# Kernel tuning notes

Measured on AMD Instinct MI355X. Metric: run time of the kernel, lower is better.

## Reference

```python
import jax, jax.numpy as jnp
import numpy as np

B = 65536      # batch size
H = 256        # hidden_size (args['hid_dim'])
MID = 300      # hard-coded encoder bottleneck in CommonFeatureExtractor
THR = 0.6      # similarity_threshold


def _lin(k, fin, fout):
    return jax.random.normal(k, (fin, fout), jnp.float32) / np.sqrt(fin)


def setup_inputs() -> dict:
    key = jax.random.key(0)
    ks = jax.random.split(key, 24)
    inp = {
        'brics': jax.random.normal(ks[0], (B, H), jnp.float32),
        'function_group': jax.random.normal(ks[1], (B, H), jnp.float32),
        'pharmacophore': jax.random.normal(ks[2], (B, H), jnp.float32),
    }
    # three fp encoders: Linear(H,300) -> ReLU -> (Dropout eval) -> Linear(300,H)
    for n, (k1, k2) in zip(['b', 'f', 'p'], [(ks[3], ks[4]), (ks[5], ks[6]), (ks[7], ks[8])]):
        inp['W1_' + n] = _lin(k1, H, MID)
        inp['b1_' + n] = jnp.zeros((MID,), jnp.float32)
        inp['W2_' + n] = _lin(k2, MID, H)
        inp['b2_' + n] = jnp.zeros((H,), jnp.float32)
    inp['Wg'] = _lin(ks[9], 3 * H, 3)        # weight_generator
    inp['bg_v'] = jnp.zeros((3,), jnp.float32)
    inp['We'] = _lin(ks[10], H, H)           # enhancement_layer
    inp['be_v'] = jnp.zeros((H,), jnp.float32)
    inp['Wf'] = _lin(ks[11], 2 * H, H)       # fusion_layer
    inp['bf_v'] = jnp.zeros((H,), jnp.float32)
    return inp


def _fwd(brics, function_group, pharmacophore,
         W1_b, b1_b, W2_b, b2_b, W1_f, b1_f, W2_f, b2_f, W1_p, b1_p, W2_p, b2_p,
         Wg, bg_v, We, be_v, Wf, bf_v):
    def enc(x, W1, b1, W2, b2):
        return jax.nn.relu(x @ W1 + b1) @ W2 + b2  # dropout in eval mode = identity

    eb = enc(brics, W1_b, b1_b, W2_b, b2_b)
    ef = enc(function_group, W1_f, b1_f, W2_f, b2_f)
    ep = enc(pharmacophore, W1_p, b1_p, W2_p, b2_p)

    fps = jnp.stack([eb, ef, ep], axis=1)                              # [B,3,H]
    fpn = fps / jnp.maximum(jnp.linalg.norm(fps, axis=-1, keepdims=True), 1e-12)

    # the 3 unordered pairs (0,1),(0,2),(1,2); the torch sort is irrelevant
    # because the selected pairs are combined by a permutation-invariant
    # softmax-weighted sum.
    ii = jnp.array([0, 0, 1])
    jj = jnp.array([1, 2, 2])
    elem = fpn[:, ii] * fpn[:, jj]                                     # [B,3,H]
    sims = elem.sum(-1)                                                # [B,3] cosine sims
    pmask = sims > THR
    common = 0.5 * (fps[:, ii] + fps[:, jj]) * (elem > THR)            # [B,3,H]

    has = pmask.any(-1)                                                # [B]
    m = jnp.max(jnp.where(pmask, sims, -jnp.inf), axis=-1, keepdims=True)
    m = jnp.where(jnp.isfinite(m), m, 0.0)
    e = jnp.where(pmask, jnp.exp(sims - m), 0.0)                       # masked softmax
    w = e / jnp.maximum(e.sum(-1, keepdims=True), 1e-12)
    sample_common = (common * w[..., None]).sum(1)                     # [B,H]
    common_features = jnp.where(has[:, None], sample_common, fps.mean(1))

    allc = jnp.concatenate([eb, ef, ep], axis=1)                       # [B,3H]
    fw = jax.nn.softmax(allc @ Wg + bg_v, axis=1)                      # [B,3]
    weighted = eb * fw[:, 0:1] + ef * fw[:, 1:2] + ep * fw[:, 2:3]

    enh = jax.nn.sigmoid(common_features @ We + be_v)
    fused = jnp.concatenate([weighted, common_features * enh], axis=1) @ Wf + bf_v
    return fused


def reference(brics, function_group, pharmacophore,
              W1_b, b1_b, W2_b, b2_b, W1_f, b1_f, W2_f, b2_f, W1_p, b1_p, W2_p, b2_p,
              Wg, bg_v, We, be_v, Wf, bf_v):
    return _fwd(brics, function_group, pharmacophore,
                W1_b, b1_b, W2_b, b2_b, W1_f, b1_f, W2_f, b2_f, W1_p, b1_p, W2_p, b2_p,
                Wg, bg_v, We, be_v, Wf, bf_v)
```

## Files before the change

kernel.cpp:

```cpp
#include <hip/hip_runtime.h>

typedef unsigned short u16;
typedef __bf16 bf16x8 __attribute__((ext_vector_type(8)));
typedef float f32x4 __attribute__((ext_vector_type(4)));
typedef unsigned short u16x8 __attribute__((ext_vector_type(8)));

__device__ __forceinline__ float b2f(u16 b){ union{unsigned u; float f;} v; v.u=((unsigned)b)<<16; return v.f; }
__device__ __forceinline__ u16 f2b(float f){ unsigned u=__builtin_bit_cast(unsigned,f); return (u16)((u+0x7fffu+((u>>16)&1u))>>16); }
__device__ __forceinline__ float wred32(float v){
  #pragma unroll
  for(int off=16; off>0; off>>=1) v += __shfl_xor(v, off, 64);
  return v;
}
__device__ __forceinline__ void stOut(u16* p, float v){ *p = f2b(v); }
__device__ __forceinline__ void stOut(float* p, float v){ *p = v; }

__device__ __forceinline__ void gload_lds16(const void* g, void* l){
  __builtin_amdgcn_global_load_lds(
      (const __attribute__((address_space(1))) void*)g,
      (__attribute__((address_space(3))) void*)l, 16, 0, 0);
}

template<int PER>
__device__ __forceinline__ void stage_tile_b16(const u16* __restrict__ base, int rstride,
                                               int kcol, u16* lds, int w, int lane){
  #pragma unroll
  for(int it=0; it<PER; ++it){
    int cbase = it*512 + w*64;
    int ch = cbase + lane;
    int r = ch >> 3;
    int ce = ((ch & 7) * 8) ^ ((r & 7) << 3);
    gload_lds16(base + (size_t)r*rstride + kcol + ce, lds + cbase*8);
  }
}

struct Af32Regs { float4 a0, b0, a1, b1; };
__device__ __forceinline__ void loadA_f32(Af32Regs& rg, const float* __restrict__ Ap,
                                          int lda, int kcol, int tid){
  {
    int ch = tid;       int r = ch>>3, s = (ch&7)*8;
    const float* src = Ap + (size_t)r*lda + kcol + s;
    rg.a0 = *(const float4*)src; rg.b0 = *(const float4*)(src+4);
  }
  {
    int ch = tid + 512; int r = ch>>3, s = (ch&7)*8;
    const float* src = Ap + (size_t)r*lda + kcol + s;
    rg.a1 = *(const float4*)src; rg.b1 = *(const float4*)(src+4);
  }
}
__device__ __forceinline__ void writeA_f32(const Af32Regs& rg, u16* As, int tid){
  {
    int ch = tid;       int r = ch>>3, s = (ch&7)*8;
    u16* dst = &As[r*64 + (s ^ ((r&7)<<3))];
    ushort4 o0{f2b(rg.a0.x),f2b(rg.a0.y),f2b(rg.a0.z),f2b(rg.a0.w)};
    ushort4 o1{f2b(rg.b0.x),f2b(rg.b0.y),f2b(rg.b0.z),f2b(rg.b0.w)};
    *(ushort4*)dst = o0; *(ushort4*)(dst+4) = o1;
  }
  {
    int ch = tid + 512; int r = ch>>3, s = (ch&7)*8;
    u16* dst = &As[r*64 + (s ^ ((r&7)<<3))];
    ushort4 o0{f2b(rg.a1.x),f2b(rg.a1.y),f2b(rg.a1.z),f2b(rg.a1.w)};
    ushort4 o1{f2b(rg.b1.x),f2b(rg.b1.y),f2b(rg.b1.z),f2b(rg.b1.w)};
    *(ushort4*)dst = o0; *(ushort4*)(dst+4) = o1;
  }
}

struct GP {
  const void* A[3];
  const void* A2;
  const u16*  Wt[3];
  const float* bias[3];
  void* C[3];
  const u16* mult;
  int lda, K, Nreal, ldc, ldm;
};

template<int MODE, typename OT, typename AT, bool DUAL, int NWT>
__global__ __launch_bounds__(512, 2) void gemm_w(GP p)
{
  const int z = blockIdx.z;
  const AT* __restrict__ A  = (const AT*)p.A[z];
  const AT* __restrict__ A2 = (const AT*)p.A2;
  const u16* __restrict__ Wt = p.Wt[z];
  const float* __restrict__ bias = p.bias[z];
  OT* __restrict__ C = (OT*)p.C[z];
  const int lda = p.lda, K = p.K, ldc = p.ldc;

  __shared__ __align__(16) u16 As[2][128*64];
  __shared__ __align__(16) u16 Bs[2][NWT*64*64];

  const int tid = threadIdx.x;
  const size_t m0 = (size_t)blockIdx.x * 128;
  const int lane = tid & 63, w = tid >> 6;
  const int lr = lane & 15, quad = lane >> 4;
  const int wr = (w >> 2) * 64, wc = (w & 3) * (NWT*16);
  const int swz = (lr & 7) << 3;
  const int KH = K >> 1, NT = K >> 6;

  f32x4 acc[4][NWT];
  #pragma unroll
  for(int i=0;i<4;++i)
    #pragma unroll
    for(int j=0;j<NWT;++j) acc[i][j] = (f32x4){0.f,0.f,0.f,0.f};

  const AT* Ab1 = A + m0*(size_t)lda;
  const AT* Ab2 = DUAL ? (A2 + m0*(size_t)lda) : nullptr;

  {
    if constexpr (__is_same(AT, u16)) {
      stage_tile_b16<2>((const u16*)Ab1, lda, 0, As[0], w, lane);
    } else {
      Af32Regs rg; loadA_f32(rg, (const float*)Ab1, lda, 0, tid);
      writeA_f32(rg, As[0], tid);
    }
    stage_tile_b16<NWT>(Wt, K, 0, Bs[0], w, lane);
  }
  __syncthreads();

  int cur = 0;
  for(int t=0; t<NT; ++t){
    const int knext = (t+1) << 6;
    const bool pf = (t+1) < NT;
    Af32Regs rg;
    if (pf){
      const AT* Ap = Ab1; int kc = knext;
      if (DUAL && knext >= KH) { Ap = Ab2; kc = knext - KH; }
      if constexpr (__is_same(AT, u16))
        stage_tile_b16<2>((const u16*)Ap, lda, kc, As[cur^1], w, lane);
      else
        loadA_f32(rg, (const float*)Ap, lda, kc, tid);
      stage_tile_b16<NWT>(Wt, K, knext, Bs[cur^1], w, lane);
    }
    #pragma unroll
    for(int kk=0; kk<64; kk+=32){
      bf16x8 af[4], bq[NWT];
      #pragma unroll
      for(int i=0;i<4;++i)
        af[i] = *(const bf16x8*)&As[cur][(wr + i*16 + lr)*64 + ((kk + quad*8) ^ swz)];
      #pragma unroll
      for(int j=0;j<NWT;++j)
        bq[j] = *(const bf16x8*)&Bs[cur][(wc + j*16 + lr)*64 + ((kk + quad*8) ^ swz)];
      #pragma unroll
      for(int i=0;i<4;++i)
        #pragma unroll
        for(int j=0;j<NWT;++j)
          acc[i][j] = __builtin_amdgcn_mfma_f32_16x16x32_bf16(af[i], bq[j], acc[i][j], 0, 0, 0);
    }
    if constexpr (!__is_same(AT, u16)) { if (pf) writeA_f32(rg, As[cur^1], tid); }
    __syncthreads();
    cur ^= 1;
  }

  #pragma unroll
  for(int j=0;j<NWT;++j){
    int col = wc + j*16 + lr;
    float bv = (col < p.Nreal) ? bias[col] : 0.f;
    #pragma unroll
    for(int i=0;i<4;++i){
      #pragma unroll
      for(int r=0;r<4;++r){
        size_t row = m0 + wr + i*16 + quad*4 + r;
        size_t ci = row*(size_t)ldc + col;
        float v = acc[i][j][r] + bv;
        if(MODE==1) v = fmaxf(v, 0.f);
        if(MODE==2){
          float mv = b2f(p.mult[row*(size_t)p.ldm + col]);
          v = mv * __builtin_amdgcn_rcpf(1.f + __expf(-v));
        }
        stOut(&C[ci], v);
      }
    }
  }
}

struct TPar { const float* src; u16* dst; int K, N, Kp, Np; };
struct TArgs { TPar p[8]; };
__global__ __launch_bounds__(256) void transpose_all(TArgs args){
  TPar p = args.p[blockIdx.y];
  int n = blockIdx.x;
  if (n >= p.Np) return;
  for (int k = threadIdx.x; k < p.Kp; k += 256){
    u16 v = 0;
    if (n < p.N && k < p.K) v = f2b(p.src[(size_t)k*p.N + n]);
    p.dst[(size_t)n*p.Kp + k] = v;
  }
}

__global__ __launch_bounds__(256) void mid_k(
    const u16* eb, const u16* ef, const u16* ep,
    const float* __restrict__ Wg, const float* __restrict__ bg,
    u16* common, u16* weighted)
{
  const int wid = threadIdx.x >> 6, lane = threadIdx.x & 63;
  const int half = lane >> 5, l5 = lane & 31;
  const size_t row = (size_t)blockIdx.x * 8 + wid*2 + half;
  const size_t base = row*256 + l5*8;

  u16x8 vb = *(const u16x8*)(eb + base);
  u16x8 vf = *(const u16x8*)(ef + base);
  u16x8 vp = *(const u16x8*)(ep + base);
  float fb[8], ff[8], fp[8];
  #pragma unroll
  for(int j=0;j<8;++j){ fb[j]=b2f(vb[j]); ff[j]=b2f(vf[j]); fp[j]=b2f(vp[j]); }

  float sb=0, sf=0, sp=0, d01=0, d02=0, d12=0, g0=0, g1=0, g2=0;
  #pragma unroll
  for(int j=0;j<8;++j){
    sb += fb[j]*fb[j]; sf += ff[j]*ff[j]; sp += fp[j]*fp[j];
    d01 += fb[j]*ff[j]; d02 += fb[j]*fp[j]; d12 += ff[j]*fp[j];
  }
  #pragma unroll
  for(int seg=0; seg<3; ++seg){
    const float* x = (seg==0) ? fb : (seg==1) ? ff : fp;
    const float* wg = Wg + ((size_t)seg*256 + l5*8)*3;
    float wv[24];
    #pragma unroll
    for(int q=0;q<6;++q){
      float4 t = *(const float4*)(wg + q*4);
      wv[q*4+0]=t.x; wv[q*4+1]=t.y; wv[q*4+2]=t.z; wv[q*4+3]=t.w;
    }
    #pragma unroll
    for(int j=0;j<8;++j){
      g0 += x[j]*wv[j*3+0];
      g1 += x[j]*wv[j*3+1];
      g2 += x[j]*wv[j*3+2];
    }
  }
  sb=wred32(sb); sf=wred32(sf); sp=wred32(sp);
  d01=wred32(d01); d02=wred32(d02); d12=wred32(d12);
  g0=wred32(g0); g1=wred32(g1); g2=wred32(g2);

  float inb  = __builtin_amdgcn_rsqf(fmaxf(sb, 1e-24f));
  float invf = __builtin_amdgcn_rsqf(fmaxf(sf, 1e-24f));
  float inp  = __builtin_amdgcn_rsqf(fmaxf(sp, 1e-24f));
  float s01 = d01*inb*invf, s02 = d02*inb*inp, s12 = d12*invf*inp;

  g0 += bg[0]; g1 += bg[1]; g2 += bg[2];
  float gm = fmaxf(g0, fmaxf(g1, g2));
  float e0 = __expf(g0-gm), e1 = __expf(g1-gm), e2 = __expf(g2-gm);
  float res = __builtin_amdgcn_rcpf(e0+e1+e2);
  float fw0 = e0*res, fw1 = e1*res, fw2 = e2*res;

  bool p0 = s01 > 0.6f, p1 = s02 > 0.6f, p2 = s12 > 0.6f;
  bool has = p0 || p1 || p2;
  float mm = -__builtin_inff();
  if(p0) mm = fmaxf(mm, s01);
  if(p1) mm = fmaxf(mm, s02);
  if(p2) mm = fmaxf(mm, s12);
  if(!has) mm = 0.f;
  float q0 = p0 ? __expf(s01-mm) : 0.f;
  float q1 = p1 ? __expf(s02-mm) : 0.f;
  float q2 = p2 ? __expf(s12-mm) : 0.f;
  float rqs = __builtin_amdgcn_rcpf(fmaxf(q0+q1+q2, 1e-12f));
  float w0 = q0*rqs, w1 = q1*rqs, w2 = q2*rqs;

  u16x8 oc, ow;
  #pragma unroll
  for(int j=0;j<8;++j){
    float a = fb[j], b = ff[j], c = fp[j];
    float na = a*inb, nbv = b*invf, nc = c*inp;
    float c0 = (na*nbv > 0.6f) ? 0.5f*(a+b) : 0.f;
    float c1 = (na*nc  > 0.6f) ? 0.5f*(a+c) : 0.f;
    float c2 = (nbv*nc > 0.6f) ? 0.5f*(b+c) : 0.f;
    float sc = c0*w0 + c1*w1 + c2*w2;
    float cf = has ? sc : (a+b+c)*(1.f/3.f);
    float wv = a*fw0 + b*fw1 + c*fw2;
    oc[j] = f2b(cf); ow[j] = f2b(wv);
  }
  *(u16x8*)(common + base) = oc;
  *(u16x8*)(weighted + base) = ow;
}

extern "C" void kernel_launch(void* const* d_in, const int* in_sizes, int n_in,
                              void* d_out, int out_size, void* d_ws, size_t ws_size,
                              hipStream_t stream) {
  const float* brics = (const float*)d_in[0];
  const float* fg    = (const float*)d_in[1];
  const float* ph    = (const float*)d_in[2];
  const float* W1[3] = {(const float*)d_in[3], (const float*)d_in[7], (const float*)d_in[11]};
  const float* b1[3] = {(const float*)d_in[4], (const float*)d_in[8], (const float*)d_in[12]};
  const float* W2[3] = {(const float*)d_in[5], (const float*)d_in[9], (const float*)d_in[13]};
  const float* b2[3] = {(const float*)d_in[6], (const float*)d_in[10], (const float*)d_in[14]};
  const float* Wg = (const float*)d_in[15];
  const float* bg = (const float*)d_in[16];
  const float* We = (const float*)d_in[17];
  const float* be = (const float*)d_in[18];
  const float* Wf = (const float*)d_in[19];
  const float* bf = (const float*)d_in[20];
  float* out = (float*)d_out;

  const int M = in_sizes[0] / 256;

  char* wsp = (char*)d_ws;
  size_t off = 0;
  auto carve = [&](size_t elems)->u16* {
    u16* p = (u16*)(wsp + off);
    off += ((elems*sizeof(u16)) + 255) & ~(size_t)255;
    return p;
  };
  u16* xb0 = carve((size_t)M*256);
  u16* xb1 = carve((size_t)M*256);
  u16* xb2 = carve((size_t)M*256);
  u16* Wt1[3], *Wt2[3];
  for(int i=0;i<3;++i) Wt1[i] = carve(320*256);
  for(int i=0;i<3;++i) Wt2[i] = carve(256*320);
  u16* WtE = carve(256*256);
  u16* WtF = carve(256*512);

  size_t hb = (((size_t)M*320*sizeof(u16)) + 255) & ~(size_t)255;
  bool batched = (off + 3*hb) <= ws_size;
  u16* hh[3];
  hh[0] = (u16*)(wsp + off);
  hh[1] = batched ? (u16*)(wsp + off + hb)   : hh[0];
  hh[2] = batched ? (u16*)(wsp + off + 2*hb) : hh[0];
  (void)n_in; (void)out_size;

  TArgs ta;
  for(int i=0;i<3;++i){
    ta.p[i]   = {W1[i], Wt1[i], 256, 300, 256, 320};
    ta.p[3+i] = {W2[i], Wt2[i], 300, 256, 320, 256};
  }
  ta.p[6] = {We, WtE, 256, 256, 256, 256};
  ta.p[7] = {Wf, WtF, 512, 256, 512, 256};
  transpose_all<<<dim3(512, 8), 256, 0, stream>>>(ta);

  const float* xin[3] = {brics, fg, ph};
  u16* encp[3] = {xb0, xb1, xb2};
  if (batched) {
    GP g1{};
    for(int i=0;i<3;++i){ g1.A[i]=xin[i]; g1.Wt[i]=Wt1[i]; g1.bias[i]=b1[i]; g1.C[i]=hh[i]; }
    g1.lda=256; g1.K=256; g1.Nreal=300; g1.ldc=320;
    gemm_w<1,u16,float,false,5><<<dim3(M/128, 1, 3), 512, 0, stream>>>(g1);
    GP g2{};
    for(int i=0;i<3;++i){ g2.A[i]=hh[i]; g2.Wt[i]=Wt2[i]; g2.bias[i]=b2[i]; g2.C[i]=encp[i]; }
    g2.lda=320; g2.K=320; g2.Nreal=256; g2.ldc=256;
    gemm_w<0,u16,u16,false,4><<<dim3(M/128, 1, 3), 512, 0, stream>>>(g2);
  } else {
    for(int i=0;i<3;++i){
      GP g1{}; g1.A[0]=xin[i]; g1.Wt[0]=Wt1[i]; g1.bias[0]=b1[i]; g1.C[0]=hh[0];
      g1.lda=256; g1.K=256; g1.Nreal=300; g1.ldc=320;
      gemm_w<1,u16,float,false,5><<<dim3(M/128, 1, 1), 512, 0, stream>>>(g1);
      GP g2{}; g2.A[0]=hh[0]; g2.Wt[0]=Wt2[i]; g2.bias[0]=b2[i]; g2.C[0]=encp[i];
      g2.lda=320; g2.K=320; g2.Nreal=256; g2.ldc=256;
      gemm_w<0,u16,u16,false,4><<<dim3(M/128, 1, 1), 512, 0, stream>>>(g2);
    }
  }

  mid_k<<<M/8, 256, 0, stream>>>(xb0, xb1, xb2, Wg, bg, xb2, xb0);

  {
    GP gg{}; gg.A[0]=xb2; gg.Wt[0]=WtE; gg.bias[0]=be; gg.C[0]=xb1;
    gg.mult=xb2; gg.lda=256; gg.K=256; gg.Nreal=256; gg.ldc=256; gg.ldm=256;
    gemm_w<2,u16,u16,false,4><<<dim3(M/128, 1, 1), 512, 0, stream>>>(gg);
  }

  {
    GP gf{}; gf.A[0]=xb0; gf.A2=xb1; gf.Wt[0]=WtF; gf.bias[0]=bf; gf.C[0]=out;
    gf.lda=256; gf.K=512; gf.Nreal=256; gf.ldc=256;
    gemm_w<0,float,u16,true,4><<<dim3(M/128, 1, 1), 512, 0, stream>>>(gf);
  }
}
```

Measured before the change: 497.5 us.

## Fuse similarity/mix, enhancement GEMM and fusion GEMM into one kernel

```diff
diff --git a/kernel.cpp b/kernel.cpp
--- a/kernel.cpp
+++ b/kernel.cpp
@@ -12,8 +12,6 @@
   for(int off=16; off>0; off>>=1) v += __shfl_xor(v, off, 64);
   return v;
 }
-__device__ __forceinline__ void stOut(u16* p, float v){ *p = f2b(v); }
-__device__ __forceinline__ void stOut(float* p, float v){ *p = v; }
 
 __device__ __forceinline__ void gload_lds16(const void* g, void* l){
   __builtin_amdgcn_global_load_lds(
@@ -67,27 +65,26 @@
 
 struct GP {
   const void* A[3];
-  const void* A2;
   const u16*  Wt[3];
   const float* bias[3];
   void* C[3];
-  const u16* mult;
-  int lda, K, Nreal, ldc, ldm;
+  int lda, K, Nreal, ldc;
 };
 
-template<int MODE, typename OT, typename AT, bool DUAL, int NWT>
+template<int MODE, typename AT, int NWT>
 __global__ __launch_bounds__(512, 2) void gemm_w(GP p)
 {
+  constexpr int BN = NWT*64;
+  constexpr int AHALF = 128*64;
+  constexpr int BHALF = BN*64;
+  __shared__ __align__(16) u16 smem[2*AHALF + 2*BHALF];
+
   const int z = blockIdx.z;
   const AT* __restrict__ A  = (const AT*)p.A[z];
-  const AT* __restrict__ A2 = (const AT*)p.A2;
   const u16* __restrict__ Wt = p.Wt[z];
   const float* __restrict__ bias = p.bias[z];
-  OT* __restrict__ C = (OT*)p.C[z];
+  u16* __restrict__ C = (u16*)p.C[z];
   const int lda = p.lda, K = p.K, ldc = p.ldc;
-
-  __shared__ __align__(16) u16 As[2][128*64];
-  __shared__ __align__(16) u16 Bs[2][NWT*64*64];
 
   const int tid = threadIdx.x;
   const size_t m0 = (size_t)blockIdx.x * 128;
@@ -95,7 +92,7 @@
   const int lr = lane & 15, quad = lane >> 4;
   const int wr = (w >> 2) * 64, wc = (w & 3) * (NWT*16);
   const int swz = (lr & 7) << 3;
-  const int KH = K >> 1, NT = K >> 6;
+  const int NT = K >> 6;
 
   f32x4 acc[4][NWT];
   #pragma unroll
@@ -103,18 +100,15 @@
     #pragma unroll
     for(int j=0;j<NWT;++j) acc[i][j] = (f32x4){0.f,0.f,0.f,0.f};
 
-  const AT* Ab1 = A + m0*(size_t)lda;
-  const AT* Ab2 = DUAL ? (A2 + m0*(size_t)lda) : nullptr;
-
-  {
-    if constexpr (__is_same(AT, u16)) {
-      stage_tile_b16<2>((const u16*)Ab1, lda, 0, As[0], w, lane);
-    } else {
-      Af32Regs rg; loadA_f32(rg, (const float*)Ab1, lda, 0, tid);
-      writeA_f32(rg, As[0], tid);
-    }
-    stage_tile_b16<NWT>(Wt, K, 0, Bs[0], w, lane);
-  }
+  const AT* Ab = A + m0*(size_t)lda;
+
+  if constexpr (__is_same(AT, u16)) {
+    stage_tile_b16<2>((const u16*)Ab, lda, 0, smem, w, lane);
+  } else {
+    Af32Regs rg; loadA_f32(rg, (const float*)Ab, lda, 0, tid);
+    writeA_f32(rg, smem, tid);
+  }
+  stage_tile_b16<NWT>(Wt, K, 0, smem + 2*AHALF, w, lane);
   __syncthreads();
 
   int cur = 0;
@@ -123,34 +117,37 @@
     const bool pf = (t+1) < NT;
     Af32Regs rg;
     if (pf){
-      const AT* Ap = Ab1; int kc = knext;
-      if (DUAL && knext >= KH) { Ap = Ab2; kc = knext - KH; }
       if constexpr (__is_same(AT, u16))
-        stage_tile_b16<2>((const u16*)Ap, lda, kc, As[cur^1], w, lane);
+        stage_tile_b16<2>((const u16*)Ab, lda, knext, smem + (cur^1)*AHALF, w, lane);
       else
-        loadA_f32(rg, (const float*)Ap, lda, kc, tid);
-      stage_tile_b16<NWT>(Wt, K, knext, Bs[cur^1], w, lane);
-    }
+        loadA_f32(rg, (const float*)Ab, lda, knext, tid);
+      stage_tile_b16<NWT>(Wt, K, knext, smem + 2*AHALF + (cur^1)*BHALF, w, lane);
+    }
+    const u16* Asc = smem + cur*AHALF;
+    const u16* Bsc = smem + 2*AHALF + cur*BHALF;
     #pragma unroll
     for(int kk=0; kk<64; kk+=32){
       bf16x8 af[4], bq[NWT];
       #pragma unroll
       for(int i=0;i<4;++i)
-        af[i] = *(const bf16x8*)&As[cur][(wr + i*16 + lr)*64 + ((kk + quad*8) ^ swz)];
+        af[i] = *(const bf16x8*)&Asc[(wr + i*16 + lr)*64 + ((kk + quad*8) ^ swz)];
       #pragma unroll
       for(int j=0;j<NWT;++j)
-        bq[j] = *(const bf16x8*)&Bs[cur][(wc + j*16 + lr)*64 + ((kk + quad*8) ^ swz)];
+        bq[j] = *(const bf16x8*)&Bsc[(wc + j*16 + lr)*64 + ((kk + quad*8) ^ swz)];
       #pragma unroll
       for(int i=0;i<4;++i)
         #pragma unroll
         for(int j=0;j<NWT;++j)
           acc[i][j] = __builtin_amdgcn_mfma_f32_16x16x32_bf16(af[i], bq[j], acc[i][j], 0, 0, 0);
     }
-    if constexpr (!__is_same(AT, u16)) { if (pf) writeA_f32(rg, As[cur^1], tid); }
+    if constexpr (!__is_same(AT, u16)) { if (pf) writeA_f32(rg, smem + (cur^1)*AHALF, tid); }
     __syncthreads();
     cur ^= 1;
   }
 
+  constexpr int BNP = BN + 8;
+  static_assert(128*BNP <= 2*AHALF + 2*BHALF, "Ct fits in smem");
+  u16* Ct = smem;
   #pragma unroll
   for(int j=0;j<NWT;++j){
     int col = wc + j*16 + lr;
@@ -159,17 +156,19 @@
     for(int i=0;i<4;++i){
       #pragma unroll
       for(int r=0;r<4;++r){
-        size_t row = m0 + wr + i*16 + quad*4 + r;
-        size_t ci = row*(size_t)ldc + col;
         float v = acc[i][j][r] + bv;
         if(MODE==1) v = fmaxf(v, 0.f);
-        if(MODE==2){
-          float mv = b2f(p.mult[row*(size_t)p.ldm + col]);
-          v = mv * __builtin_amdgcn_rcpf(1.f + __expf(-v));
-        }
-        stOut(&C[ci], v);
+        Ct[(wr + i*16 + quad*4 + r)*BNP + col] = f2b(v);
       }
     }
+  }
+  __syncthreads();
+  const int rowg = tid >> 2, cg = tid & 3;
+  const size_t crow = (m0 + rowg)*(size_t)ldc;
+  #pragma unroll
+  for(int k2=0; k2<BN/32; ++k2){
+    int c = (cg + k2*4)*8;
+    *(u16x8*)&C[crow + c] = *(const u16x8*)&Ct[rowg*BNP + c];
   }
 }
 
@@ -186,89 +185,202 @@
   }
 }
 
-__global__ __launch_bounds__(256) void mid_k(
-    const u16* eb, const u16* ef, const u16* ep,
+__global__ __launch_bounds__(512, 2) void fuse3_k(
+    const u16* __restrict__ eb, const u16* __restrict__ ef, const u16* __restrict__ ep,
     const float* __restrict__ Wg, const float* __restrict__ bg,
-    u16* common, u16* weighted)
+    const u16* __restrict__ WtE, const float* __restrict__ be,
+    const u16* __restrict__ WtF, const float* __restrict__ bfv,
+    float* __restrict__ out)
 {
-  const int wid = threadIdx.x >> 6, lane = threadIdx.x & 63;
-  const int half = lane >> 5, l5 = lane & 31;
-  const size_t row = (size_t)blockIdx.x * 8 + wid*2 + half;
-  const size_t base = row*256 + l5*8;
-
-  u16x8 vb = *(const u16x8*)(eb + base);
-  u16x8 vf = *(const u16x8*)(ef + base);
-  u16x8 vp = *(const u16x8*)(ep + base);
-  float fb[8], ff[8], fp[8];
-  #pragma unroll
-  for(int j=0;j<8;++j){ fb[j]=b2f(vb[j]); ff[j]=b2f(vf[j]); fp[j]=b2f(vp[j]); }
-
-  float sb=0, sf=0, sp=0, d01=0, d02=0, d12=0, g0=0, g1=0, g2=0;
-  #pragma unroll
-  for(int j=0;j<8;++j){
-    sb += fb[j]*fb[j]; sf += ff[j]*ff[j]; sp += fp[j]*fp[j];
-    d01 += fb[j]*ff[j]; d02 += fb[j]*fp[j]; d12 += ff[j]*fp[j];
-  }
-  #pragma unroll
-  for(int seg=0; seg<3; ++seg){
-    const float* x = (seg==0) ? fb : (seg==1) ? ff : fp;
-    const float* wg = Wg + ((size_t)seg*256 + l5*8)*3;
-    float wv[24];
-    #pragma unroll
-    for(int q=0;q<6;++q){
-      float4 t = *(const float4*)(wg + q*4);
-      wv[q*4+0]=t.x; wv[q*4+1]=t.y; wv[q*4+2]=t.z; wv[q*4+3]=t.w;
-    }
+  constexpr int BHALF = 256*64;
+  __shared__ __align__(16) u16 cw[4*64*64];
+  __shared__ __align__(16) u16 ww[4*64*64];
+  __shared__ __align__(16) u16 Bst[2*BHALF];
+
+  const int tid = threadIdx.x;
+  const size_t m0 = (size_t)blockIdx.x * 64;
+  const int lane = tid & 63, w = tid >> 6;
+  const int lr = lane & 15, quad = lane >> 4;
+  const int wr = (w >> 2) * 32, wc = (w & 3) * 64;
+  const int swz = (lr & 7) << 3;
+
+  stage_tile_b16<4>(WtE, 256, 0, Bst, w, lane);
+
+  const int rid = tid >> 5, l5 = tid & 31;
+  for(int pass=0; pass<4; ++pass){
+    int rloc = pass*16 + rid;
+    size_t base = (m0 + rloc)*256 + l5*8;
+
+    u16x8 vb = *(const u16x8*)(eb + base);
+    u16x8 vf = *(const u16x8*)(ef + base);
+    u16x8 vp = *(const u16x8*)(ep + base);
+    float fb[8], ff[8], fp[8];
+    #pragma unroll
+    for(int j=0;j<8;++j){ fb[j]=b2f(vb[j]); ff[j]=b2f(vf[j]); fp[j]=b2f(vp[j]); }
+
+    float sb=0, sf=0, sp=0, d01=0, d02=0, d12=0, g0=0, g1=0, g2=0;
     #pragma unroll
     for(int j=0;j<8;++j){
-      g0 += x[j]*wv[j*3+0];
-      g1 += x[j]*wv[j*3+1];
-      g2 += x[j]*wv[j*3+2];
-    }
-  }
-  sb=wred32(sb); sf=wred32(sf); sp=wred32(sp);
-  d01=wred32(d01); d02=wred32(d02); d12=wred32(d12);
-  g0=wred32(g0); g1=wred32(g1); g2=wred32(g2);
-
-  float inb  = __builtin_amdgcn_rsqf(fmaxf(sb, 1e-24f));
-  float invf = __builtin_amdgcn_rsqf(fmaxf(sf, 1e-24f));
-  float inp  = __builtin_amdgcn_rsqf(fmaxf(sp, 1e-24f));
-  float s01 = d01*inb*invf, s02 = d02*inb*inp, s12 = d12*invf*inp;
-
-  g0 += bg[0]; g1 += bg[1]; g2 += bg[2];
-  float gm = fmaxf(g0, fmaxf(g1, g2));
-  float e0 = __expf(g0-gm), e1 = __expf(g1-gm), e2 = __expf(g2-gm);
-  float res = __builtin_amdgcn_rcpf(e0+e1+e2);
-  float fw0 = e0*res, fw1 = e1*res, fw2 = e2*res;
-
-  bool p0 = s01 > 0.6f, p1 = s02 > 0.6f, p2 = s12 > 0.6f;
-  bool has = p0 || p1 || p2;
-  float mm = -__builtin_inff();
-  if(p0) mm = fmaxf(mm, s01);
-  if(p1) mm = fmaxf(mm, s02);
-  if(p2) mm = fmaxf(mm, s12);
-  if(!has) mm = 0.f;
-  float q0 = p0 ? __expf(s01-mm) : 0.f;
-  float q1 = p1 ? __expf(s02-mm) : 0.f;
-  float q2 = p2 ? __expf(s12-mm) : 0.f;
-  float rqs = __builtin_amdgcn_rcpf(fmaxf(q0+q1+q2, 1e-12f));
-  float w0 = q0*rqs, w1 = q1*rqs, w2 = q2*rqs;
-
-  u16x8 oc, ow;
-  #pragma unroll
-  for(int j=0;j<8;++j){
-    float a = fb[j], b = ff[j], c = fp[j];
-    float na = a*inb, nbv = b*invf, nc = c*inp;
-    float c0 = (na*nbv > 0.6f) ? 0.5f*(a+b) : 0.f;
-    float c1 = (na*nc  > 0.6f) ? 0.5f*(a+c) : 0.f;
-    float c2 = (nbv*nc > 0.6f) ? 0.5f*(b+c) : 0.f;
-    float sc = c0*w0 + c1*w1 + c2*w2;
-    float cf = has ? sc : (a+b+c)*(1.f/3.f);
-    float wv = a*fw0 + b*fw1 + c*fw2;
-    oc[j] = f2b(cf); ow[j] = f2b(wv);
-  }
-  *(u16x8*)(common + base) = oc;
-  *(u16x8*)(weighted + base) = ow;
+      sb += fb[j]*fb[j]; sf += ff[j]*ff[j]; sp += fp[j]*fp[j];
+      d01 += fb[j]*ff[j]; d02 += fb[j]*fp[j]; d12 += ff[j]*fp[j];
+    }
+    #pragma unroll
+    for(int seg=0; seg<3; ++seg){
+      const float* x = (seg==0) ? fb : (seg==1) ? ff : fp;
+      const float* wg = Wg + ((size_t)seg*256 + l5*8)*3;
+      float wv[24];
+      #pragma unroll
+      for(int q=0;q<6;++q){
+        float4 t = *(const float4*)(wg + q*4);
+        wv[q*4+0]=t.x; wv[q*4+1]=t.y; wv[q*4+2]=t.z; wv[q*4+3]=t.w;
+      }
+      #pragma unroll
+      for(int j=0;j<8;++j){
+        g0 += x[j]*wv[j*3+0];
+        g1 += x[j]*wv[j*3+1];
+        g2 += x[j]*wv[j*3+2];
+      }
+    }
+    sb=wred32(sb); sf=wred32(sf); sp=wred32(sp);
+    d01=wred32(d01); d02=wred32(d02); d12=wred32(d12);
+    g0=wred32(g0); g1=wred32(g1); g2=wred32(g2);
+
+    float inb  = __builtin_amdgcn_rsqf(fmaxf(sb, 1e-24f));
+    float invf = __builtin_amdgcn_rsqf(fmaxf(sf, 1e-24f));
+    float inp  = __builtin_amdgcn_rsqf(fmaxf(sp, 1e-24f));
+    float s01 = d01*inb*invf, s02 = d02*inb*inp, s12 = d12*invf*inp;
+
+    float h0 = g0 + bg[0], h1 = g1 + bg[1], h2 = g2 + bg[2];
+    float gm = fmaxf(h0, fmaxf(h1, h2));
+    float e0 = __expf(h0-gm), e1 = __expf(h1-gm), e2 = __expf(h2-gm);
+    float res = __builtin_amdgcn_rcpf(e0+e1+e2);
+    float fw0 = e0*res, fw1 = e1*res, fw2 = e2*res;
+
+    bool p0 = s01 > 0.6f, p1 = s02 > 0.6f, p2 = s12 > 0.6f;
+    bool has = p0 || p1 || p2;
+    float mm = -__builtin_inff();
+    if(p0) mm = fmaxf(mm, s01);
+    if(p1) mm = fmaxf(mm, s02);
+    if(p2) mm = fmaxf(mm, s12);
+    if(!has) mm = 0.f;
+    float q0 = p0 ? __expf(s01-mm) : 0.f;
+    float q1 = p1 ? __expf(s02-mm) : 0.f;
+    float q2 = p2 ? __expf(s12-mm) : 0.f;
+    float rqs = __builtin_amdgcn_rcpf(fmaxf(q0+q1+q2, 1e-12f));
+    float w0 = q0*rqs, w1 = q1*rqs, w2 = q2*rqs;
+
+    u16x8 oc, ow;
+    #pragma unroll
+    for(int j=0;j<8;++j){
+      float a = fb[j], b = ff[j], c = fp[j];
+      float na = a*inb, nbv = b*invf, nc = c*inp;
+      float c0 = (na*nbv > 0.6f) ? 0.5f*(a+b) : 0.f;
+      float c1 = (na*nc  > 0.6f) ? 0.5f*(a+c) : 0.f;
+      float c2 = (nbv*nc > 0.6f) ? 0.5f*(b+c) : 0.f;
+      float sc = c0*w0 + c1*w1 + c2*w2;
+      float cf = has ? sc : (a+b+c)*(1.f/3.f);
+      float wv = a*fw0 + b*fw1 + c*fw2;
+      oc[j] = f2b(cf); ow[j] = f2b(wv);
+    }
+    int idx = (l5>>3)*4096 + rloc*64 + (((l5&7)*8) ^ ((rloc&7)<<3));
+    *(u16x8*)&cw[idx] = oc;
+    *(u16x8*)&ww[idx] = ow;
+  }
+  __syncthreads();
+
+  f32x4 ga[2][4];
+  #pragma unroll
+  for(int i=0;i<2;++i)
+    #pragma unroll
+    for(int j=0;j<4;++j) ga[i][j] = (f32x4){0.f,0.f,0.f,0.f};
+
+  int cur = 0;
+  for(int t=0; t<4; ++t){
+    if(t<3) stage_tile_b16<4>(WtE, 256, (t+1)*64, Bst + (cur^1)*BHALF, w, lane);
+    const u16* Asc = cw + t*4096;
+    const u16* Bsc = Bst + cur*BHALF;
+    #pragma unroll
+    for(int kk=0; kk<64; kk+=32){
+      bf16x8 af[2], bq[4];
+      #pragma unroll
+      for(int i=0;i<2;++i)
+        af[i] = *(const bf16x8*)&Asc[(wr + i*16 + lr)*64 + ((kk + quad*8) ^ swz)];
+      #pragma unroll
+      for(int j=0;j<4;++j)
+        bq[j] = *(const bf16x8*)&Bsc[(wc + j*16 + lr)*64 + ((kk + quad*8) ^ swz)];
+      #pragma unroll
+      for(int i=0;i<2;++i)
+        #pragma unroll
+        for(int j=0;j<4;++j)
+          ga[i][j] = __builtin_amdgcn_mfma_f32_16x16x32_bf16(af[i], bq[j], ga[i][j], 0, 0, 0);
+    }
+    __syncthreads();
+    cur ^= 1;
+  }
+  stage_tile_b16<4>(WtF, 512, 0, Bst, w, lane);
+
+  #pragma unroll
+  for(int j=0;j<4;++j){
+    int col = wc + j*16 + lr;
+    float bev = be[col];
+    int within = j*16 + lr;
+    #pragma unroll
+    for(int i=0;i<2;++i){
+      #pragma unroll
+      for(int r=0;r<4;++r){
+        int rl = wr + i*16 + quad*4 + r;
+        int idx = (w & 3)*4096 + rl*64 + (within ^ ((rl&7)<<3));
+        float cv = b2f(cw[idx]);
+        float v = ga[i][j][r] + bev;
+        cw[idx] = f2b(cv * __builtin_amdgcn_rcpf(1.f + __expf(-v)));
+      }
+    }
+  }
+  __syncthreads();
+
+  f32x4 fa[2][4];
+  #pragma unroll
+  for(int i=0;i<2;++i)
+    #pragma unroll
+    for(int j=0;j<4;++j) fa[i][j] = (f32x4){0.f,0.f,0.f,0.f};
+
+  cur = 0;
+  for(int t=0; t<8; ++t){
+    if(t<7) stage_tile_b16<4>(WtF, 512, (t+1)*64, Bst + (cur^1)*BHALF, w, lane);
+    const u16* Asc = (t < 4) ? (ww + t*4096) : (cw + (t-4)*4096);
+    const u16* Bsc = Bst + cur*BHALF;
+    #pragma unroll
+    for(int kk=0; kk<64; kk+=32){
+      bf16x8 af[2], bq[4];
+      #pragma unroll
+      for(int i=0;i<2;++i)
+        af[i] = *(const bf16x8*)&Asc[(wr + i*16 + lr)*64 + ((kk + quad*8) ^ swz)];
+      #pragma unroll
+      for(int j=0;j<4;++j)
+        bq[j] = *(const bf16x8*)&Bsc[(wc + j*16 + lr)*64 + ((kk + quad*8) ^ swz)];
+      #pragma unroll
+      for(int i=0;i<2;++i)
+        #pragma unroll
+        for(int j=0;j<4;++j)
+          fa[i][j] = __builtin_amdgcn_mfma_f32_16x16x32_bf16(af[i], bq[j], fa[i][j], 0, 0, 0);
+    }
+    __syncthreads();
+    cur ^= 1;
+  }
+
+  #pragma unroll
+  for(int j=0;j<4;++j){
+    int col = wc + j*16 + lr;
+    float bfc = bfv[col];
+    #pragma unroll
+    for(int i=0;i<2;++i){
+      #pragma unroll
+      for(int r=0;r<4;++r){
+        size_t row = m0 + wr + i*16 + quad*4 + r;
+        out[row*256 + col] = fa[i][j][r] + bfc;
+      }
+    }
+  }
 }
 
 extern "C" void kernel_launch(void* const* d_in, const int* in_sizes, int n_in,
@@ -330,33 +442,21 @@
     GP g1{};
     for(int i=0;i<3;++i){ g1.A[i]=xin[i]; g1.Wt[i]=Wt1[i]; g1.bias[i]=b1[i]; g1.C[i]=hh[i]; }
     g1.lda=256; g1.K=256; g1.Nreal=300; g1.ldc=320;
-    gemm_w<1,u16,float,false,5><<<dim3(M/128, 1, 3), 512, 0, stream>>>(g1);
+    gemm_w<1,float,5><<<dim3(M/128, 1, 3), 512, 0, stream>>>(g1);
     GP g2{};
     for(int i=0;i<3;++i){ g2.A[i]=hh[i]; g2.Wt[i]=Wt2[i]; g2.bias[i]=b2[i]; g2.C[i]=encp[i]; }
     g2.lda=320; g2.K=320; g2.Nreal=256; g2.ldc=256;
-    gemm_w<0,u16,u16,false,4><<<dim3(M/128, 1, 3), 512, 0, stream>>>(g2);
+    gemm_w<0,u16,4><<<dim3(M/128, 1, 3), 512, 0, stream>>>(g2);
   } else {
     for(int i=0;i<3;++i){
       GP g1{}; g1.A[0]=xin[i]; g1.Wt[0]=Wt1[i]; g1.bias[0]=b1[i]; g1.C[0]=hh[0];
       g1.lda=256; g1.K=256; g1.Nreal=300; g1.ldc=320;
-      gemm_w<1,u16,float,false,5><<<dim3(M/128, 1, 1), 512, 0, stream>>>(g1);
+      gemm_w<1,float,5><<<dim3(M/128, 1, 1), 512, 0, stream>>>(g1);
       GP g2{}; g2.A[0]=hh[0]; g2.Wt[0]=Wt2[i]; g2.bias[0]=b2[i]; g2.C[0]=encp[i];
       g2.lda=320; g2.K=320; g2.Nreal=256; g2.ldc=256;
-      gemm_w<0,u16,u16,false,4><<<dim3(M/128, 1, 1), 512, 0, stream>>>(g2);
-    }
-  }
-
-  mid_k<<<M/8, 256, 0, stream>>>(xb0, xb1, xb2, Wg, bg, xb2, xb0);
-
-  {
-    GP gg{}; gg.A[0]=xb2; gg.Wt[0]=WtE; gg.bias[0]=be; gg.C[0]=xb1;
-    gg.mult=xb2; gg.lda=256; gg.K=256; gg.Nreal=256; gg.ldc=256; gg.ldm=256;
-    gemm_w<2,u16,u16,false,4><<<dim3(M/128, 1, 1), 512, 0, stream>>>(gg);
-  }
-
-  {
-    GP gf{}; gf.A[0]=xb0; gf.A2=xb1; gf.Wt[0]=WtF; gf.bias[0]=bf; gf.C[0]=out;
-    gf.lda=256; gf.K=512; gf.Nreal=256; gf.ldc=256;
-    gemm_w<0,float,u16,true,4><<<dim3(M/128, 1, 1), 512, 0, stream>>>(gf);
-  }
-}
+      gemm_w<0,u16,4><<<dim3(M/128, 1, 1), 512, 0, stream>>>(g2);
+    }
+  }
+
+  fuse3_k<<<M/64, 512, 0, stream>>>(xb0, xb1, xb2, Wg, bg, WtE, be, WtF, bf, out);
+}
```

New measurement: 434.4 us. 12.7% less time.
